# Kernel tuning notes

Hardware: AMD Instinct MI355X
Metric: run time of the kernel (lower is better)

## Reference

```python
import jax, jax.numpy as jnp
import numpy as np
import math


def haar_dwt(x):
    # x: [B, C, H, W] -> (LL [B,C,H/2,W/2], bands [B,C,3,H/2,W/2]) orthogonal Haar
    B, C, H, W = x.shape
    xr = x.reshape(B, C, H // 2, 2, W // 2, 2)
    a = xr[:, :, :, 0, :, 0]
    b = xr[:, :, :, 0, :, 1]
    c = xr[:, :, :, 1, :, 0]
    d = xr[:, :, :, 1, :, 1]
    ll = (a + b + c + d) * 0.5
    lh = (a + b - c - d) * 0.5  # horizontal detail
    hl = (a - b + c - d) * 0.5  # vertical detail
    hh = (a - b - c + d) * 0.5  # diagonal detail
    return ll, jnp.stack([lh, hl, hh], axis=2)


def haar_idwt(ll, bands):
    # inverse of haar_dwt (perfect reconstruction)
    lh, hl, hh = bands[:, :, 0], bands[:, :, 1], bands[:, :, 2]
    a = (ll + lh + hl + hh) * 0.5
    b = (ll + lh - hl - hh) * 0.5
    c = (ll - lh + hl - hh) * 0.5
    d = (ll - lh - hl + hh) * 0.5
    B, C, h, w = ll.shape
    out = jnp.stack([jnp.stack([a, b], -1), jnp.stack([c, d], -1)], -3)  # [B,C,h,2,w,2]
    return out.reshape(B, C, 2 * h, 2 * w)


def selective_scan(u, prompt, x_proj_w, dt_proj_w, dt_proj_b, A_logs, Ds):
    # u: [B, L, C] input sequence; prompt: [B, L, N] added to C projection
    B, L, C = u.shape
    R = dt_proj_w.shape[1]
    N = A_logs.shape[1]
    x_dbl = jnp.einsum('blc,rc->blr', u, x_proj_w)            # [B, L, R+2N]
    dts, Bs, Cs = jnp.split(x_dbl, [R, R + N], axis=-1)        # [B,L,R], [B,L,N], [B,L,N]
    delta = jax.nn.softplus(jnp.einsum('blr,cr->blc', dts, dt_proj_w) + dt_proj_b)  # [B,L,C]
    Cs = Cs + prompt
    A = -jnp.exp(A_logs)                                       # [C, N]
    # time-major for scan
    delta_t = jnp.moveaxis(delta, 1, 0)                        # [L,B,C]
    u_t = jnp.moveaxis(u, 1, 0)                                # [L,B,C]
    Bs_t = jnp.moveaxis(Bs, 1, 0)                              # [L,B,N]
    Cs_t = jnp.moveaxis(Cs, 1, 0)                              # [L,B,N]
    dA = jnp.exp(delta_t[..., None] * A)                       # [L,B,C,N]
    dBu = delta_t[..., None] * Bs_t[:, :, None, :] * u_t[..., None]  # [L,B,C,N]

    def step(h, inp):
        dA_l, dBu_l, C_l = inp
        h = dA_l * h + dBu_l
        y = jnp.einsum('bcn,bn->bc', h, C_l)
        return h, y

    h0 = jnp.zeros((B, C, N), dtype=u.dtype)
    _, ys = jax.lax.scan(step, h0, (dA, dBu, Cs_t))            # ys: [L,B,C]
    y = jnp.moveaxis(ys, 0, 1)                                 # [B,L,C]
    return y + u * Ds


def setup_inputs() -> dict:
    B, H, W, C, N = 4, 128, 128, 128, 8
    R = math.ceil(C / 16)  # dt_rank = 8
    L = H * W
    key = jax.random.key(0)
    ks = jax.random.split(key, 10)
    x = jax.random.normal(ks[0], (B, L, C), jnp.float32)
    prompt = jax.random.normal(ks[1], (B, L, N), jnp.float32) * 0.1
    in_proj_w = jax.random.normal(ks[2], (2 * C, C), jnp.float32) * (C ** -0.5)
    x_proj_w = jax.random.normal(ks[3], (R + 2 * N, C), jnp.float32) * (C ** -0.5)
    std = R ** -0.5
    dt_proj_w = jax.random.uniform(ks[4], (C, R), jnp.float32, minval=-std, maxval=std)
    dt = jnp.clip(jnp.exp(jax.random.uniform(ks[5], (C,), jnp.float32)
                          * (math.log(0.1) - math.log(0.001)) + math.log(0.001)), 1e-4)
    dt_proj_b = dt + jnp.log(-jnp.expm1(-dt))  # inverse softplus init
    A_logs = jnp.broadcast_to(jnp.log(jnp.arange(1, N + 1, dtype=jnp.float32)), (C, N)).copy()
    Ds = jnp.ones((C,), jnp.float32)
    ln_gamma = jnp.ones((C,), jnp.float32)
    ln_beta = jnp.zeros((C,), jnp.float32)
    out_proj_w = jax.random.normal(ks[6], (C, C), jnp.float32) * (C ** -0.5)
    out_proj_b = jnp.zeros((C,), jnp.float32)
    return dict(x=x, prompt=prompt, in_proj_w=in_proj_w, x_proj_w=x_proj_w,
                dt_proj_w=dt_proj_w, dt_proj_b=dt_proj_b, A_logs=A_logs, Ds=Ds,
                ln_gamma=ln_gamma, ln_beta=ln_beta, out_proj_w=out_proj_w,
                out_proj_b=out_proj_b, H=H, W=W)


def reference(x, prompt, in_proj_w, x_proj_w, dt_proj_w, dt_proj_b, A_logs, Ds,
              ln_gamma, ln_beta, out_proj_w, out_proj_b, H, W):
    B, L, C = x.shape
    xz = x @ in_proj_w.T                                       # [B,L,2C]
    x_proc, z = jnp.split(xz, 2, axis=-1)
    prepare = x_proc.reshape(B, H, W, C).transpose(0, 3, 1, 2)  # [B,C,H,W]
    # J=2 Haar DWT
    Yl1, bands1 = haar_dwt(prepare)                            # level 1: H/2
    Yl2, bands2 = haar_dwt(Yl1)                                # level 2: H/4
    h2, w2 = H // 4, W // 4
    # pack coarsest level into top-left quadrants of a zero canvas (as original)
    h00 = jnp.zeros_like(prepare)
    h00 = h00.at[:, :, :h2, :w2].set(Yl2)
    h00 = h00.at[:, :, :h2, w2:2 * w2].set(bands2[:, :, 0])
    h00 = h00.at[:, :, h2:2 * h2, :w2].set(bands2[:, :, 1])
    h00 = h00.at[:, :, h2:2 * h2, w2:2 * w2].set(bands2[:, :, 2])
    h00_seq = h00.transpose(0, 2, 3, 1).reshape(B, L, C)
    # Mamba-style selective scan over the wavelet-domain sequence
    h11_seq = selective_scan(h00_seq, prompt, x_proj_w, dt_proj_w, dt_proj_b, A_logs, Ds)
    h11 = h11_seq.reshape(B, H, W, C).transpose(0, 3, 1, 2)
    # unpack scanned coarsest level; level-1 details kept as-is
    Yl2n = h11[:, :, :h2, :w2]
    bands2n = jnp.stack([h11[:, :, :h2, w2:2 * w2],
                         h11[:, :, h2:2 * h2, :w2],
                         h11[:, :, h2:2 * h2, w2:2 * w2]], axis=2)
    Yl1n = haar_idwt(Yl2n, bands2n)
    recons = haar_idwt(Yl1n, bands1)                           # [B,C,H,W]
    y = recons.transpose(0, 2, 3, 1).reshape(B, L, C)
    # LayerNorm over channels
    mu = jnp.mean(y, axis=-1, keepdims=True)
    var = jnp.var(y, axis=-1, keepdims=True)
    y = (y - mu) * jax.lax.rsqrt(var + 1e-5) * ln_gamma + ln_beta
    # SiLU gate + output projection + residual
    y = y * jax.nn.silu(z)
    out = y @ out_proj_w.T + out_proj_b
    return out + x
```

## Files before the change

kernel.cpp:

```cpp
#include <hip/hip_runtime.h>

#define B_   4
#define H_   128
#define W_   128
#define L_   (H_*W_)
#define C_   128
#define N_   8
#define R_   8
#define LS_  4096
#define CS_  16
#define NC_  256
#define ST_  (B_*LS_)

#define OFF_XPROC 0ull
#define OFF_Z     (OFF_XPROC + (size_t)B_*L_*C_)
#define OFF_BANDS (OFF_Z     + (size_t)B_*L_*C_)
#define OFF_U     (OFF_BANDS + (size_t)B_*3*64*64*C_)
#define OFF_DELTA (OFF_U     + (size_t)B_*LS_*C_)
#define OFF_BS    (OFF_DELTA + (size_t)B_*LS_*C_)
#define OFF_CS    (OFF_BS    + (size_t)B_*LS_*N_)
#define OFF_DSUM  (OFF_CS    + (size_t)B_*LS_*N_)
#define OFF_HEND  (OFF_DSUM  + (size_t)B_*NC_*C_)
#define OFF_HIN   (OFF_HEND  + (size_t)B_*NC_*C_*N_)
#define OFF_H11   (OFF_HIN   + (size_t)B_*NC_*C_*N_)
#define OFF_XDBL  (OFF_H11   + (size_t)B_*LS_*C_)
#define OFF_WCVT  (OFF_XDBL  + (size_t)ST_*32)

typedef __attribute__((ext_vector_type(8))) short bf16x8;
typedef __attribute__((ext_vector_type(4))) float f32x4;

__device__ __forceinline__ float softplus_f(float x) {
    return (x > 20.f) ? x : log1pf(__expf(x));
}

__device__ __forceinline__ void split_bf16(float x, short& h, short& l) {
    const unsigned u  = __float_as_uint(x);
    const unsigned hr = (u + 0x7FFFu + ((u >> 16) & 1u)) >> 16;
    h = (short)hr;
    const float hf = __uint_as_float(hr << 16);
    l = (short)(__float_as_uint(x - hf) >> 16);
}

__device__ __forceinline__ f32x4 mfma16(bf16x8 a, bf16x8 b, f32x4 c) {
    return __builtin_amdgcn_mfma_f32_16x16x32_bf16(a, b, c, 0, 0, 0);
}

__global__ __launch_bounds__(256) void k_cvt(const float* __restrict__ w_in,
        const float* __restrict__ w_out, const float* __restrict__ xw,
        unsigned short* __restrict__ wq) {
    const int i = blockIdx.x * 256 + threadIdx.x;
    float v; unsigned short *hi, *lo; int idx;
    if (i < 32768)      { v = w_in[i];          hi = wq;         lo = wq + 32768;  idx = i; }
    else if (i < 49152) { v = w_out[i - 32768]; hi = wq + 65536; lo = wq + 81920;  idx = i - 32768; }
    else {
        idx = i - 49152;
        v = (idx < 24*128) ? xw[idx] : 0.f;
        hi = wq + 98304; lo = wq + 102400;
    }
    short h, l; split_bf16(v, h, l);
    hi[idx] = (unsigned short)h;
    lo[idx] = (unsigned short)l;
}

template<bool EPI>
__global__ __launch_bounds__(256) void k_gemm_mfma(const float* __restrict__ in,
        const unsigned short* __restrict__ whi, const unsigned short* __restrict__ wlo,
        float* __restrict__ out0, float* __restrict__ out1,
        const float* __restrict__ bias, const float* __restrict__ resid) {
    const int tid  = threadIdx.x;
    const int wave = tid >> 6, lane = tid & 63;
    const int lrow = lane & 15;
    const int lk8  = (lane >> 4) << 3;
    int r0, c0;
    if constexpr (EPI) { r0 = blockIdx.x * 64 + (wave >> 1) * 32; c0 = (wave & 1) * 64; }
    else               { r0 = blockIdx.x * 32;                    c0 = wave * 64; }

    f32x4 acc[2][4];
    #pragma unroll
    for (int rb = 0; rb < 2; ++rb)
        #pragma unroll
        for (int cb = 0; cb < 4; ++cb)
            acc[rb][cb] = (f32x4){0.f, 0.f, 0.f, 0.f};

    const float* a0 = in + (size_t)(r0 + lrow) * C_ + lk8;
    const float* a1 = in + (size_t)(r0 + 16 + lrow) * C_ + lk8;

    #pragma unroll
    for (int ks = 0; ks < 4; ++ks) {
        bf16x8 ah[2], al[2];
        #pragma unroll
        for (int rb = 0; rb < 2; ++rb) {
            const float* ap = (rb ? a1 : a0) + ks * 32;
            const float4 v0 = *(const float4*)ap;
            const float4 v1 = *(const float4*)(ap + 4);
            const float f[8] = {v0.x, v0.y, v0.z, v0.w, v1.x, v1.y, v1.z, v1.w};
            #pragma unroll
            for (int i = 0; i < 8; ++i) {
                short h, l; split_bf16(f[i], h, l);
                ah[rb][i] = h; al[rb][i] = l;
            }
        }
        #pragma unroll
        for (int cb = 0; cb < 4; ++cb) {
            const size_t boff = (size_t)(c0 + cb * 16 + lrow) * C_ + ks * 32 + lk8;
            const bf16x8 bh = *(const bf16x8*)(whi + boff);
            const bf16x8 bl = *(const bf16x8*)(wlo + boff);
            #pragma unroll
            for (int rb = 0; rb < 2; ++rb) {
                f32x4 t = acc[rb][cb];
                t = mfma16(ah[rb], bh, t);
                t = mfma16(ah[rb], bl, t);
                t = mfma16(al[rb], bh, t);
                acc[rb][cb] = t;
            }
        }
    }
    #pragma unroll
    for (int rb = 0; rb < 2; ++rb)
        #pragma unroll
        for (int cb = 0; cb < 4; ++cb) {
            const int col = c0 + cb * 16 + lrow;
            float* op; int colo;
            if constexpr (EPI) { op = out0; colo = col; }
            else { const bool toz = (c0 + cb * 16) >= 128; op = toz ? out1 : out0; colo = col & 127; }
            const float bz = EPI ? bias[colo] : 0.f;
            #pragma unroll
            for (int j = 0; j < 4; ++j) {
                const size_t row = (size_t)r0 + rb * 16 + (lane >> 4) * 4 + j;
                float v = acc[rb][cb][j] + bz;
                if constexpr (EPI) v += resid[row * C_ + colo];
                op[row * C_ + colo] = v;
            }
        }
}

__global__ __launch_bounds__(256) void k_xdbl(const float* __restrict__ u,
        const unsigned short* __restrict__ xwhi, const unsigned short* __restrict__ xwlo,
        float* __restrict__ xd) {
    const int tid  = threadIdx.x;
    const int wave = tid >> 6, lane = tid & 63;
    const int lrow = lane & 15;
    const int lk8  = (lane >> 4) << 3;
    const int r0   = blockIdx.x * 128 + wave * 32;

    f32x4 acc[2][2];
    #pragma unroll
    for (int rb = 0; rb < 2; ++rb)
        #pragma unroll
        for (int cb = 0; cb < 2; ++cb)
            acc[rb][cb] = (f32x4){0.f, 0.f, 0.f, 0.f};

    const float* a0 = u + (size_t)(r0 + lrow) * C_ + lk8;
    const float* a1 = u + (size_t)(r0 + 16 + lrow) * C_ + lk8;

    #pragma unroll
    for (int ks = 0; ks < 4; ++ks) {
        bf16x8 ah[2], al[2];
        #pragma unroll
        for (int rb = 0; rb < 2; ++rb) {
            const float* ap = (rb ? a1 : a0) + ks * 32;
            const float4 v0 = *(const float4*)ap;
            const float4 v1 = *(const float4*)(ap + 4);
            const float f[8] = {v0.x, v0.y, v0.z, v0.w, v1.x, v1.y, v1.z, v1.w};
            #pragma unroll
            for (int i = 0; i < 8; ++i) {
                short h, l; split_bf16(f[i], h, l);
                ah[rb][i] = h; al[rb][i] = l;
            }
        }
        #pragma unroll
        for (int cb = 0; cb < 2; ++cb) {
            const size_t boff = (size_t)(cb * 16 + lrow) * C_ + ks * 32 + lk8;
            const bf16x8 bh = *(const bf16x8*)(xwhi + boff);
            const bf16x8 bl = *(const bf16x8*)(xwlo + boff);
            #pragma unroll
            for (int rb = 0; rb < 2; ++rb) {
                f32x4 t = acc[rb][cb];
                t = mfma16(ah[rb], bh, t);
                t = mfma16(ah[rb], bl, t);
                t = mfma16(al[rb], bh, t);
                acc[rb][cb] = t;
            }
        }
    }
    #pragma unroll
    for (int rb = 0; rb < 2; ++rb)
        #pragma unroll
        for (int cb = 0; cb < 2; ++cb) {
            const int col = cb * 16 + lrow;
            #pragma unroll
            for (int j = 0; j < 4; ++j) {
                const int row = r0 + rb * 16 + (lane >> 4) * 4 + j;
                xd[(size_t)row * 32 + col] = acc[rb][cb][j];
            }
        }
}

__global__ __launch_bounds__(256) void k_dbc(const float* __restrict__ xd,
        const float* __restrict__ prompt, const float* __restrict__ dtw,
        const float* __restrict__ dtb, float* __restrict__ delta,
        float* __restrict__ Bsv, float* __restrict__ Csv) {
    const int tid = threadIdx.x;
    const int g = blockIdx.x * 2 + (tid >> 7);
    const int c = tid & 127;
    const float* xr = xd + (size_t)g * 32;
    float wreg[8];
    *(float4*)&wreg[0] = *(const float4*)(dtw + c*8);
    *(float4*)&wreg[4] = *(const float4*)(dtw + c*8 + 4);
    float dd = dtb[c];
    #pragma unroll
    for (int r = 0; r < 8; ++r) dd += xr[r] * wreg[r];
    delta[(size_t)g * C_ + c] = softplus_f(dd);
    if (c < 8) {
        Bsv[(size_t)g * N_ + c] = xr[8 + c];
    } else if (c < 16) {
        const int n = c - 8;
        const int b = g >> 12, s = g & 4095;
        const int l = ((s >> 6) << 7) | (s & 63);
        Csv[(size_t)g * N_ + n] = xr[16 + n] + prompt[((size_t)b*L_ + l)*N_ + n];
    }
}

__global__ __launch_bounds__(128) void k_dwt(const float* __restrict__ xp,
        float* __restrict__ bands, float* __restrict__ u) {
    const int c = threadIdx.x;
    const int bid = blockIdx.x;
    const int b = bid >> 10, p = (bid >> 5) & 31, q = bid & 31;
    float v[4][4];
    const size_t base = (size_t)b * L_ * C_ + c;
    #pragma unroll
    for (int i = 0; i < 4; ++i)
        #pragma unroll
        for (int j = 0; j < 4; ++j)
            v[i][j] = xp[base + (size_t)(((p<<2)+i)*W_ + (q<<2)+j) * C_];
    const size_t bstride = (size_t)64*64*C_;
    float ll[2][2];
    #pragma unroll
    for (int di = 0; di < 2; ++di)
        #pragma unroll
        for (int dj = 0; dj < 2; ++dj) {
            const float a  = v[2*di][2*dj],   bb = v[2*di][2*dj+1];
            const float cc = v[2*di+1][2*dj], dd = v[2*di+1][2*dj+1];
            ll[di][dj]     = (a+bb+cc+dd)*0.5f;
            const float lh = (a+bb-cc-dd)*0.5f;
            const float hl = (a-bb+cc-dd)*0.5f;
            const float hh = (a-bb-cc+dd)*0.5f;
            const int i1 = (p<<1)+di, j1 = (q<<1)+dj;
            const size_t bb0 = (((size_t)b*3*64 + i1)*64 + j1)*C_ + c;
            bands[bb0]             = lh;
            bands[bb0 +   bstride] = hl;
            bands[bb0 + 2*bstride] = hh;
        }
    const float a = ll[0][0], bb = ll[0][1], cc = ll[1][0], dd = ll[1][1];
    const float l2  = (a+bb+cc+dd)*0.5f;
    const float lh2 = (a+bb-cc-dd)*0.5f;
    const float hl2 = (a-bb+cc-dd)*0.5f;
    const float hh2 = (a-bb-cc+dd)*0.5f;
    const size_t ub = (size_t)b*LS_*C_ + c;
    u[ub + (size_t)((p<<6)+q)*C_]          = l2;
    u[ub + (size_t)((p<<6)+32+q)*C_]       = lh2;
    u[ub + (size_t)(((32+p)<<6)+q)*C_]     = hl2;
    u[ub + (size_t)(((32+p)<<6)+32+q)*C_]  = hh2;
}

__global__ __launch_bounds__(256) void k_scan1(const float* __restrict__ delta,
        const float* __restrict__ u, const float* __restrict__ Bsv,
        const float* __restrict__ Alog, float* __restrict__ dsum, float* __restrict__ hend) {
    const int tid = threadIdx.x;
    const int b = blockIdx.x >> 7, k2 = blockIdx.x & 127;
    const int k = (k2 << 1) | (tid >> 7);
    const int c = tid & 127;
    float al[8];
    *(float4*)&al[0] = *(const float4*)(Alog + c*8);
    *(float4*)&al[4] = *(const float4*)(Alog + c*8 + 4);
    float an[8];
    #pragma unroll
    for (int n = 0; n < 8; ++n) an[n] = -__expf(al[n]);
    float h[8] = {0,0,0,0,0,0,0,0};
    float cum = 0.f;
    const int s0 = k << 4;
    for (int t = 0; t < CS_; ++t) {
        const int s = s0 + t;
        const size_t base = ((size_t)b*LS_ + s)*C_ + c;
        const float d  = delta[base];
        const float uu = u[base];
        float bv[8];
        const float4* bp = (const float4*)(Bsv + ((size_t)b*LS_ + s)*N_);
        *(float4*)&bv[0] = bp[0];
        *(float4*)&bv[4] = bp[1];
        cum += d;
        const float du = d * uu;
        #pragma unroll
        for (int n = 0; n < 8; ++n)
            h[n] = __expf(d*an[n])*h[n] + bv[n]*du;
    }
    const size_t idx = (size_t)(b*NC_ + k)*C_ + c;
    dsum[idx] = cum;
    *(float4*)(hend + idx*N_)     = make_float4(h[0],h[1],h[2],h[3]);
    *(float4*)(hend + idx*N_ + 4) = make_float4(h[4],h[5],h[6],h[7]);
}

#define KB_ 16
__global__ __launch_bounds__(256) void k_comb(const float* __restrict__ dsum,
        const float* __restrict__ hend, const float* __restrict__ Alog,
        const float* __restrict__ dtb, float* __restrict__ hin) {
    const int g = blockIdx.x * 256 + threadIdx.x;
    const int b = g >> 10;
    const int c = (g >> 3) & 127;
    const int n = g & 7;
    const float a  = -__expf(Alog[c*N_ + n]);
    const float d0 = softplus_f(dtb[c]);
    const float dz = __expf(a * (64.f * d0));
    float carry = 0.f;
    float ea[KB_], ha[KB_], eb[KB_], hb[KB_];
    auto LOAD = [&](int kb, float* e, float* hv) {
        #pragma unroll
        for (int j = 0; j < KB_; ++j) {
            const size_t idx = (size_t)(b*NC_ + kb + j)*C_ + c;
            e[j]  = a * dsum[idx];
            hv[j] = hend[idx*N_ + n];
        }
    };
    auto CHAIN = [&](int kb, const float* e, const float* hv) {
        #pragma unroll
        for (int j = 0; j < KB_; ++j) {
            const int k = kb + j;
            if (k && !(k & 3)) carry *= dz;
            hin[((size_t)(b*NC_ + k)*C_ + c)*N_ + n] = carry;
            carry = __expf(e[j])*carry + hv[j];
        }
    };
    LOAD(0, ea, ha);
    for (int kb = 0; kb < NC_; kb += 2*KB_) {
        LOAD(kb + KB_, eb, hb);
        CHAIN(kb, ea, ha);
        if (kb + 2*KB_ < NC_) LOAD(kb + 2*KB_, ea, ha);
        CHAIN(kb + KB_, eb, hb);
    }
}

__global__ __launch_bounds__(256) void k_scan2(const float* __restrict__ delta,
        const float* __restrict__ u, const float* __restrict__ Bsv,
        const float* __restrict__ Csv, const float* __restrict__ Alog,
        const float* __restrict__ Ds, const float* __restrict__ hin,
        float* __restrict__ h11) {
    const int tid = threadIdx.x;
    const int b = blockIdx.x >> 7, k2 = blockIdx.x & 127;
    const int k = (k2 << 1) | (tid >> 7);
    const int c = tid & 127;
    float al[8];
    *(float4*)&al[0] = *(const float4*)(Alog + c*8);
    *(float4*)&al[4] = *(const float4*)(Alog + c*8 + 4);
    float an[8];
    #pragma unroll
    for (int n = 0; n < 8; ++n) an[n] = -__expf(al[n]);
    float h[8];
    const float4* hp = (const float4*)(hin + ((size_t)(b*NC_ + k)*C_ + c)*N_);
    *(float4*)&h[0] = hp[0];
    *(float4*)&h[4] = hp[1];
    const float dsc = Ds[c];
    const int s0 = k << 4;
    for (int t = 0; t < CS_; ++t) {
        const int s = s0 + t;
        const size_t base = ((size_t)b*LS_ + s)*C_ + c;
        const float d  = delta[base];
        const float uu = u[base];
        float bv[8], cv[8];
        const float4* bp = (const float4*)(Bsv + ((size_t)b*LS_ + s)*N_);
        const float4* cp = (const float4*)(Csv + ((size_t)b*LS_ + s)*N_);
        *(float4*)&bv[0] = bp[0];
        *(float4*)&bv[4] = bp[1];
        *(float4*)&cv[0] = cp[0];
        *(float4*)&cv[4] = cp[1];
        const float du = d * uu;
        float y = uu * dsc;
        #pragma unroll
        for (int n = 0; n < 8; ++n) {
            h[n] = __expf(d*an[n])*h[n] + bv[n]*du;
            y += h[n] * cv[n];
        }
        h11[base] = y;
    }
}

__global__ __launch_bounds__(128) void k_idwt_ln(const float* __restrict__ h11,
        const float* __restrict__ bands, const float* __restrict__ z,
        const float* __restrict__ gamma, const float* __restrict__ beta,
        float* __restrict__ yout) {
    __shared__ float vb[16][129];
    __shared__ float stat[16][2];
    const int c = threadIdx.x;
    const int bid = blockIdx.x;
    const int b = bid >> 10, p = (bid >> 5) & 31, q = bid & 31;
    const size_t ub = (size_t)b*LS_*C_ + c;
    const float l2  = h11[ub + (size_t)((p<<6)+q)*C_];
    const float lh2 = h11[ub + (size_t)((p<<6)+32+q)*C_];
    const float hl2 = h11[ub + (size_t)(((32+p)<<6)+q)*C_];
    const float hh2 = h11[ub + (size_t)(((32+p)<<6)+32+q)*C_];
    float yl1[2][2];
    yl1[0][0] = (l2+lh2+hl2+hh2)*0.5f;
    yl1[0][1] = (l2+lh2-hl2-hh2)*0.5f;
    yl1[1][0] = (l2-lh2+hl2-hh2)*0.5f;
    yl1[1][1] = (l2-lh2-hl2+hh2)*0.5f;
    const size_t bstride = (size_t)64*64*C_;
    float v[16];
    #pragma unroll
    for (int di = 0; di < 2; ++di)
        #pragma unroll
        for (int dj = 0; dj < 2; ++dj) {
            const int i1 = (p<<1)+di, j1 = (q<<1)+dj;
            const size_t bb0 = (((size_t)b*3*64 + i1)*64 + j1)*C_ + c;
            const float lh = bands[bb0];
            const float hl = bands[bb0 +   bstride];
            const float hh = bands[bb0 + 2*bstride];
            const float ll = yl1[di][dj];
            v[(2*di+0)*4 + 2*dj+0] = (ll+lh+hl+hh)*0.5f;
            v[(2*di+0)*4 + 2*dj+1] = (ll+lh-hl-hh)*0.5f;
            v[(2*di+1)*4 + 2*dj+0] = (ll-lh+hl-hh)*0.5f;
            v[(2*di+1)*4 + 2*dj+1] = (ll-lh-hl+hh)*0.5f;
        }
    #pragma unroll
    for (int p16 = 0; p16 < 16; ++p16) vb[p16][c] = v[p16];
    __syncthreads();
    {
        const int pp = c >> 3, gg = c & 7;
        float s = 0.f, ss = 0.f;
        #pragma unroll
        for (int i = 0; i < 16; ++i) {
            const float x = vb[pp][gg*16 + i];
            s += x; ss += x*x;
        }
        s += __shfl_xor(s, 1); ss += __shfl_xor(ss, 1);
        s += __shfl_xor(s, 2); ss += __shfl_xor(ss, 2);
        s += __shfl_xor(s, 4); ss += __shfl_xor(ss, 4);
        if (gg == 0) { stat[pp][0] = s; stat[pp][1] = ss; }
    }
    __syncthreads();
    const float gm = gamma[c], bt = beta[c];
    #pragma unroll
    for (int p16 = 0; p16 < 16; ++p16) {
        const int lr = p16 >> 2, lc = p16 & 3;
        const size_t l = (size_t)((p<<2)+lr)*W_ + (q<<2)+lc;
        const float mu  = stat[p16][0] * 0.0078125f;
        const float var = stat[p16][1] * 0.0078125f - mu*mu;
        const float ri  = rsqrtf(var + 1e-5f);
        float y = (v[p16] - mu)*ri*gm + bt;
        const float zv = z[((size_t)b*L_ + l)*C_ + c];
        y *= zv / (1.f + __expf(-zv));
        yout[((size_t)b*L_ + l)*C_ + c] = y;
    }
}

extern "C" void kernel_launch(void* const* d_in, const int* in_sizes, int n_in,
                              void* d_out, int out_size, void* d_ws, size_t ws_size,
                              hipStream_t stream) {
    (void)in_sizes; (void)n_in; (void)out_size; (void)ws_size;
    const float* x      = (const float*)d_in[0];
    const float* prompt = (const float*)d_in[1];
    const float* in_w   = (const float*)d_in[2];
    const float* x_w    = (const float*)d_in[3];
    const float* dt_w   = (const float*)d_in[4];
    const float* dt_b   = (const float*)d_in[5];
    const float* A_logs = (const float*)d_in[6];
    const float* Ds     = (const float*)d_in[7];
    const float* gam    = (const float*)d_in[8];
    const float* bet    = (const float*)d_in[9];
    const float* out_w  = (const float*)d_in[10];
    const float* out_b  = (const float*)d_in[11];
    float* wsp   = (float*)d_ws;
    float* xproc = wsp + OFF_XPROC;
    float* z     = wsp + OFF_Z;
    float* bands = wsp + OFF_BANDS;
    float* u     = wsp + OFF_U;
    float* delta = wsp + OFF_DELTA;
    float* Bs    = wsp + OFF_BS;
    float* Cs    = wsp + OFF_CS;
    float* dsum  = wsp + OFF_DSUM;
    float* hend  = wsp + OFF_HEND;
    float* hin   = wsp + OFF_HIN;
    float* h11   = wsp + OFF_H11;
    float* xd    = wsp + OFF_XDBL;
    unsigned short* wq = (unsigned short*)(wsp + OFF_WCVT);
    unsigned short* whi_in  = wq;
    unsigned short* wlo_in  = wq + 32768;
    unsigned short* whi_out = wq + 65536;
    unsigned short* wlo_out = wq + 81920;
    unsigned short* whi_xw  = wq + 98304;
    unsigned short* wlo_xw  = wq + 102400;
    float* out   = (float*)d_out;

    k_cvt<<<208, 256, 0, stream>>>(in_w, out_w, x_w, wq);
    k_gemm_mfma<false><<<2048, 256, 0, stream>>>(x, whi_in, wlo_in, xproc, z, nullptr, nullptr);
    k_dwt<<<4096, 128, 0, stream>>>(xproc, bands, u);
    k_xdbl<<<128, 256, 0, stream>>>(u, whi_xw, wlo_xw, xd);
    k_dbc<<<8192, 256, 0, stream>>>(xd, prompt, dt_w, dt_b, delta, Bs, Cs);
    k_scan1<<<512, 256, 0, stream>>>(delta, u, Bs, A_logs, dsum, hend);
    k_comb<<<16, 256, 0, stream>>>(dsum, hend, A_logs, dt_b, hin);
    k_scan2<<<512, 256, 0, stream>>>(delta, u, Bs, Cs, A_logs, Ds, hin, h11);
    k_idwt_ln<<<4096, 128, 0, stream>>>(h11, bands, z, gam, bet, xproc);
    k_gemm_mfma<true><<<1024, 256, 0, stream>>>(xproc, whi_out, wlo_out, out, nullptr, out_b, x);
}
```

Before: 258.0 us.

## Make projection GEMMs persistent with register-resident weights and vectorized epilogue

```diff
diff --git a/kernel.cpp b/kernel.cpp
--- a/kernel.cpp
+++ b/kernel.cpp
@@ -63,7 +63,7 @@
 }
 
 template<bool EPI>
-__global__ __launch_bounds__(256) void k_gemm_mfma(const float* __restrict__ in,
+__global__ __launch_bounds__(256, 2) void k_gemm2(const float* __restrict__ in,
         const unsigned short* __restrict__ whi, const unsigned short* __restrict__ wlo,
         float* __restrict__ out0, float* __restrict__ out1,
         const float* __restrict__ bias, const float* __restrict__ resid) {
@@ -71,67 +71,81 @@
     const int wave = tid >> 6, lane = tid & 63;
     const int lrow = lane & 15;
     const int lk8  = (lane >> 4) << 3;
-    int r0, c0;
-    if constexpr (EPI) { r0 = blockIdx.x * 64 + (wave >> 1) * 32; c0 = (wave & 1) * 64; }
-    else               { r0 = blockIdx.x * 32;                    c0 = wave * 64; }
-
-    f32x4 acc[2][4];
-    #pragma unroll
-    for (int rb = 0; rb < 2; ++rb)
-        #pragma unroll
-        for (int cb = 0; cb < 4; ++cb)
-            acc[rb][cb] = (f32x4){0.f, 0.f, 0.f, 0.f};
-
-    const float* a0 = in + (size_t)(r0 + lrow) * C_ + lk8;
-    const float* a1 = in + (size_t)(r0 + 16 + lrow) * C_ + lk8;
-
-    #pragma unroll
-    for (int ks = 0; ks < 4; ++ks) {
-        bf16x8 ah[2], al[2];
+    const int oc4  = (lane >> 4) << 2;
+
+    int c0, wr;
+    if constexpr (EPI) { c0 = (wave & 1) * 64; wr = wave >> 1; }
+    else               { c0 = wave * 64;       wr = 0; }
+
+    bf16x8 Bh[4][4], Bl[4][4];
+    #pragma unroll
+    for (int cb = 0; cb < 4; ++cb)
+        #pragma unroll
+        for (int ks = 0; ks < 4; ++ks) {
+            const size_t boff = (size_t)(c0 + cb * 16 + lrow) * C_ + ks * 32 + lk8;
+            Bh[cb][ks] = *(const bf16x8*)(whi + boff);
+            Bl[cb][ks] = *(const bf16x8*)(wlo + boff);
+        }
+
+    const int nch = EPI ? 1024 : 2048;
+    for (int ch = blockIdx.x; ch < nch; ch += gridDim.x) {
+        const int r0 = EPI ? (ch * 64 + wr * 32) : ch * 32;
+        f32x4 acc[2][4];
+        #pragma unroll
+        for (int rb = 0; rb < 2; ++rb)
+            #pragma unroll
+            for (int cb = 0; cb < 4; ++cb)
+                acc[rb][cb] = (f32x4){0.f, 0.f, 0.f, 0.f};
+
         #pragma unroll
         for (int rb = 0; rb < 2; ++rb) {
-            const float* ap = (rb ? a1 : a0) + ks * 32;
-            const float4 v0 = *(const float4*)ap;
-            const float4 v1 = *(const float4*)(ap + 4);
-            const float f[8] = {v0.x, v0.y, v0.z, v0.w, v1.x, v1.y, v1.z, v1.w};
-            #pragma unroll
-            for (int i = 0; i < 8; ++i) {
-                short h, l; split_bf16(f[i], h, l);
-                ah[rb][i] = h; al[rb][i] = l;
+            const float* ap = in + (size_t)(r0 + rb * 16 + lrow) * C_;
+            float4 ar[8];
+            #pragma unroll
+            for (int ks = 0; ks < 4; ++ks) {
+                ar[2*ks]   = *(const float4*)(ap + ks * 32 + lk8);
+                ar[2*ks+1] = *(const float4*)(ap + ks * 32 + lk8 + 4);
             }
-        }
-        #pragma unroll
-        for (int cb = 0; cb < 4; ++cb) {
-            const size_t boff = (size_t)(c0 + cb * 16 + lrow) * C_ + ks * 32 + lk8;
-            const bf16x8 bh = *(const bf16x8*)(whi + boff);
-            const bf16x8 bl = *(const bf16x8*)(wlo + boff);
-            #pragma unroll
-            for (int rb = 0; rb < 2; ++rb) {
-                f32x4 t = acc[rb][cb];
-                t = mfma16(ah[rb], bh, t);
-                t = mfma16(ah[rb], bl, t);
-                t = mfma16(al[rb], bh, t);
-                acc[rb][cb] = t;
+            #pragma unroll
+            for (int ks = 0; ks < 4; ++ks) {
+                const float f[8] = {ar[2*ks].x, ar[2*ks].y, ar[2*ks].z, ar[2*ks].w,
+                                    ar[2*ks+1].x, ar[2*ks+1].y, ar[2*ks+1].z, ar[2*ks+1].w};
+                bf16x8 ah, al;
+                #pragma unroll
+                for (int i = 0; i < 8; ++i) {
+                    short h, l; split_bf16(f[i], h, l);
+                    ah[i] = h; al[i] = l;
+                }
+                #pragma unroll
+                for (int cb = 0; cb < 4; ++cb) {
+                    f32x4 t = acc[rb][cb];
+                    t = mfma16(Bh[cb][ks], ah, t);
+                    t = mfma16(Bl[cb][ks], ah, t);
+                    t = mfma16(Bh[cb][ks], al, t);
+                    acc[rb][cb] = t;
+                }
             }
         }
-    }
-    #pragma unroll
-    for (int rb = 0; rb < 2; ++rb)
-        #pragma unroll
-        for (int cb = 0; cb < 4; ++cb) {
-            const int col = c0 + cb * 16 + lrow;
-            float* op; int colo;
-            if constexpr (EPI) { op = out0; colo = col; }
-            else { const bool toz = (c0 + cb * 16) >= 128; op = toz ? out1 : out0; colo = col & 127; }
-            const float bz = EPI ? bias[colo] : 0.f;
-            #pragma unroll
-            for (int j = 0; j < 4; ++j) {
-                const size_t row = (size_t)r0 + rb * 16 + (lane >> 4) * 4 + j;
-                float v = acc[rb][cb][j] + bz;
-                if constexpr (EPI) v += resid[row * C_ + colo];
-                op[row * C_ + colo] = v;
+        #pragma unroll
+        for (int rb = 0; rb < 2; ++rb) {
+            const size_t row = (size_t)r0 + rb * 16 + lrow;
+            #pragma unroll
+            for (int cb = 0; cb < 4; ++cb) {
+                const int col = c0 + cb * 16 + oc4;
+                f32x4 v = acc[rb][cb];
+                if constexpr (EPI) {
+                    const float4 bz = *(const float4*)(bias + col);
+                    const float4 rv = *(const float4*)(resid + row * C_ + col);
+                    v[0] += bz.x + rv.x; v[1] += bz.y + rv.y;
+                    v[2] += bz.z + rv.z; v[3] += bz.w + rv.w;
+                    *(f32x4*)(out0 + row * C_ + col) = v;
+                } else {
+                    float* op = (c0 >= 128) ? out1 : out0;
+                    *(f32x4*)(op + row * C_ + (col & 127)) = v;
+                }
             }
         }
+    }
 }
 
 __global__ __launch_bounds__(256) void k_xdbl(const float* __restrict__ u,
@@ -490,7 +504,7 @@
     float* out   = (float*)d_out;
 
     k_cvt<<<208, 256, 0, stream>>>(in_w, out_w, x_w, wq);
-    k_gemm_mfma<false><<<2048, 256, 0, stream>>>(x, whi_in, wlo_in, xproc, z, nullptr, nullptr);
+    k_gemm2<false><<<512, 256, 0, stream>>>(x, whi_in, wlo_in, xproc, z, nullptr, nullptr);
     k_dwt<<<4096, 128, 0, stream>>>(xproc, bands, u);
     k_xdbl<<<128, 256, 0, stream>>>(u, whi_xw, wlo_xw, xd);
     k_dbc<<<8192, 256, 0, stream>>>(xd, prompt, dt_w, dt_b, delta, Bs, Cs);
@@ -498,5 +512,5 @@
     k_comb<<<16, 256, 0, stream>>>(dsum, hend, A_logs, dt_b, hin);
     k_scan2<<<512, 256, 0, stream>>>(delta, u, Bs, Cs, A_logs, Ds, hin, h11);
     k_idwt_ln<<<4096, 128, 0, stream>>>(h11, bands, z, gam, bet, xproc);
-    k_gemm_mfma<true><<<1024, 256, 0, stream>>>(xproc, whi_out, wlo_out, out, nullptr, out_b, x);
-}
+    k_gemm2<true><<<512, 256, 0, stream>>>(xproc, whi_out, wlo_out, out, nullptr, out_b, x);
+}
```

Measured after the change: 232.0 us. 1.11x faster.
